# Kernel optimization log

Measured on AMD Instinct MI355X. Metric: run time of the kernel, lower is better.

## Reference

```python
import jax, jax.numpy as jnp
import numpy as np

B, QS, KS = 8, 1024, 1024
QDIM = KDIM = VDIM = 512
HEADS, ODIM = 8, 64
NEG_SLOPE = 0.2


def setup_inputs() -> dict:
    key = jax.random.key(0)
    ks = jax.random.split(key, 7)
    return {
        "Q": jax.random.normal(ks[0], (B, QS, QDIM), jnp.float32),
        "K": jax.random.normal(ks[1], (B, KS, KDIM), jnp.float32),
        "V": jax.random.normal(ks[2], (B, KS, VDIM), jnp.float32),
        # torch Linear weights: (out_features, in_features)
        "WQ": jax.random.normal(ks[3], (HEADS, QDIM), jnp.float32) * 0.05,
        "WK": jax.random.normal(ks[4], (HEADS, KDIM), jnp.float32) * 0.05,
        "WV": jax.random.normal(ks[5], (HEADS * ODIM, VDIM), jnp.float32) * 0.05,
        "bias": jax.random.normal(ks[6], (HEADS, ODIM), jnp.float32) * 0.05,
    }


def reference(Q, K, V, WQ, WK, WV, bias):
    b, qs = Q.shape[:2]
    Vproj = (V @ WV.T).reshape(b, -1, HEADS, ODIM)          # (b, k, h, d)
    attn_K = K @ WK.T                                        # (b, k, h)
    attn_Q = Q @ WQ.T                                        # (b, q, h)
    # additive GAT-style scores: (b, q, k, h)
    w = jax.nn.leaky_relu(attn_Q[:, :, None, :] + attn_K[:, None, :, :],
                          negative_slope=NEG_SLOPE)
    w = jax.nn.softmax(w, axis=2)                            # softmax over keys
    out = jnp.einsum('bqkh,bkhd->bqhd', w, Vproj) + bias     # (b, q, h, d)
    return out.reshape(b, qs, -1)
```

## Files before the change

kernel.cpp:

```cpp
#include <hip/hip_runtime.h>
#include <hip/hip_bf16.h>

#define NS 0.2f


typedef _Float16 half8 __attribute__((ext_vector_type(8)));
typedef float f32x4 __attribute__((ext_vector_type(4)));

__global__ __launch_bounds__(256) void projQK_kernel(
    const float* __restrict__ Q, const float* __restrict__ K,
    const float* __restrict__ WQ, const float* __restrict__ WK,
    float* __restrict__ aQ, float* __restrict__ aK) {
  int bid = blockIdx.x;
  const float* X;
  const float* W;
  float* aX;
  int rb;
  if (bid < 512) { X = Q; W = WQ; aX = aQ; rb = bid; }
  else           { X = K; W = WK; aX = aK; rb = bid - 512; }
  __shared__ __align__(16) float Wl[8 * 512];
  int t = threadIdx.x;
#pragma unroll
  for (int i = 0; i < 16; i++) Wl[i * 256 + t] = W[i * 256 + t];
  __syncthreads();
  int w = t >> 6, lane = t & 63;
#pragma unroll
  for (int r = 0; r < 4; r++) {
    int row = rb * 16 + w * 4 + r;
    const float* x = X + (size_t)row * 512;
    float4 x0 = *(const float4*)(x + lane * 4);
    float4 x1 = *(const float4*)(x + 256 + lane * 4);
    float acc[8];
#pragma unroll
    for (int h = 0; h < 8; h++) {
      const float* wl = Wl + h * 512;
      float4 w0 = *(const float4*)(wl + lane * 4);
      float4 w1 = *(const float4*)(wl + 256 + lane * 4);
      float a = x0.x * w0.x + x0.y * w0.y + x0.z * w0.z + x0.w * w0.w +
                x1.x * w1.x + x1.y * w1.y + x1.z * w1.z + x1.w * w1.w;
#pragma unroll
      for (int off = 32; off > 0; off >>= 1) a += __shfl_xor(a, off);
      acc[h] = a;
    }
    if (lane == 0) {
      float* o = aX + (size_t)row * 8;
      o[0] = acc[0]; o[1] = acc[1]; o[2] = acc[2]; o[3] = acc[3];
      o[4] = acc[4]; o[5] = acc[5]; o[6] = acc[6]; o[7] = acc[7];
    }
  }
}

__global__ __launch_bounds__(256) void vproj_mfma(
    const float* __restrict__ A, const float* __restrict__ Wv,
    _Float16* __restrict__ C) {
  __shared__ __align__(16) _Float16 As[64 * 64];
  __shared__ __align__(16) _Float16 Bs[64 * 64];
  int t = threadIdx.x;
  int m0 = blockIdx.x * 64, n0 = blockIdx.y * 64;
  int lane = t & 63, wid = t >> 6;
  int wr = wid >> 1, wc = wid & 1;
  int sr = t >> 2, sc = t & 3;
  const float* ap = A + (size_t)(m0 + sr) * 512 + sc * 16;
  const float* bp = Wv + (size_t)(n0 + sr) * 512 + sc * 16;
  int swz = sr & 7;
  _Float16* aw0 = As + sr * 64 + (((2 * sc + 0) ^ swz) * 8);
  _Float16* aw1 = As + sr * 64 + (((2 * sc + 1) ^ swz) * 8);
  _Float16* bw0 = Bs + sr * 64 + (((2 * sc + 0) ^ swz) * 8);
  _Float16* bw1 = Bs + sr * 64 + (((2 * sc + 1) ^ swz) * 8);
  int fr = lane & 15, fs = lane >> 4;
  f32x4 acc[2][2];
#pragma unroll
  for (int i = 0; i < 2; i++)
#pragma unroll
    for (int j = 0; j < 2; j++)
#pragma unroll
      for (int r = 0; r < 4; r++) acc[i][j][r] = 0.f;

  float4 a0 = *(const float4*)(ap);
  float4 a1 = *(const float4*)(ap + 4);
  float4 a2 = *(const float4*)(ap + 8);
  float4 a3 = *(const float4*)(ap + 12);
  float4 b0 = *(const float4*)(bp);
  float4 b1 = *(const float4*)(bp + 4);
  float4 b2 = *(const float4*)(bp + 8);
  float4 b3 = *(const float4*)(bp + 12);
  for (int k0 = 0; k0 < 512; k0 += 64) {
    half8 ah0, ah1, bh0, bh1;
    ah0[0] = (_Float16)a0.x; ah0[1] = (_Float16)a0.y;
    ah0[2] = (_Float16)a0.z; ah0[3] = (_Float16)a0.w;
    ah0[4] = (_Float16)a1.x; ah0[5] = (_Float16)a1.y;
    ah0[6] = (_Float16)a1.z; ah0[7] = (_Float16)a1.w;
    ah1[0] = (_Float16)a2.x; ah1[1] = (_Float16)a2.y;
    ah1[2] = (_Float16)a2.z; ah1[3] = (_Float16)a2.w;
    ah1[4] = (_Float16)a3.x; ah1[5] = (_Float16)a3.y;
    ah1[6] = (_Float16)a3.z; ah1[7] = (_Float16)a3.w;
    bh0[0] = (_Float16)b0.x; bh0[1] = (_Float16)b0.y;
    bh0[2] = (_Float16)b0.z; bh0[3] = (_Float16)b0.w;
    bh0[4] = (_Float16)b1.x; bh0[5] = (_Float16)b1.y;
    bh0[6] = (_Float16)b1.z; bh0[7] = (_Float16)b1.w;
    bh1[0] = (_Float16)b2.x; bh1[1] = (_Float16)b2.y;
    bh1[2] = (_Float16)b2.z; bh1[3] = (_Float16)b2.w;
    bh1[4] = (_Float16)b3.x; bh1[5] = (_Float16)b3.y;
    bh1[6] = (_Float16)b3.z; bh1[7] = (_Float16)b3.w;
    if (k0 + 64 < 512) {
      a0 = *(const float4*)(ap + k0 + 64);
      a1 = *(const float4*)(ap + k0 + 68);
      a2 = *(const float4*)(ap + k0 + 72);
      a3 = *(const float4*)(ap + k0 + 76);
      b0 = *(const float4*)(bp + k0 + 64);
      b1 = *(const float4*)(bp + k0 + 68);
      b2 = *(const float4*)(bp + k0 + 72);
      b3 = *(const float4*)(bp + k0 + 76);
    }
    __syncthreads();
    *(half8*)aw0 = ah0;
    *(half8*)aw1 = ah1;
    *(half8*)bw0 = bh0;
    *(half8*)bw1 = bh1;
    __syncthreads();
    half8 af[2][2], bf[2][2];
#pragma unroll
    for (int i = 0; i < 2; i++) {
      int R = wr * 32 + i * 16 + fr;
#pragma unroll
      for (int kk = 0; kk < 2; kk++)
        af[i][kk] = *(half8*)(As + R * 64 + (((fs + 4 * kk) ^ (R & 7)) * 8));
    }
#pragma unroll
    for (int j = 0; j < 2; j++) {
      int Cc = wc * 32 + j * 16 + fr;
#pragma unroll
      for (int kk = 0; kk < 2; kk++)
        bf[j][kk] = *(half8*)(Bs + Cc * 64 + (((fs + 4 * kk) ^ (Cc & 7)) * 8));
    }
#pragma unroll
    for (int i = 0; i < 2; i++)
#pragma unroll
      for (int j = 0; j < 2; j++) {
        acc[i][j] = __builtin_amdgcn_mfma_f32_16x16x32_f16(
            af[i][0], bf[j][0], acc[i][j], 0, 0, 0);
        acc[i][j] = __builtin_amdgcn_mfma_f32_16x16x32_f16(
            af[i][1], bf[j][1], acc[i][j], 0, 0, 0);
      }
  }
#pragma unroll
  for (int i = 0; i < 2; i++)
#pragma unroll
    for (int j = 0; j < 2; j++) {
      int row = m0 + wr * 32 + i * 16 + fs * 4;
      int col = n0 + wc * 32 + j * 16 + fr;
#pragma unroll
      for (int r = 0; r < 4; r++)
        C[(size_t)(row + r) * 512 + col] = (_Float16)acc[i][j][r];
    }
}

__global__ __launch_bounds__(1024) void sortbin_kernel(
    const float* __restrict__ aK, const float* __restrict__ aQ,
    const _Float16* __restrict__ Vp, float* __restrict__ E1g,
    float* __restrict__ E2g, int* __restrict__ IDXg,
    float* __restrict__ cofs1, float* __restrict__ cofs2,
    float* __restrict__ scof1, float* __restrict__ scof2,
    float* __restrict__ amaxArr, int* __restrict__ binStart,
    int* __restrict__ binData, float* __restrict__ binX) {
  int bh = blockIdx.x, b = bh >> 3, h = bh & 7;
  __shared__ float key[1024];
  __shared__ int idx[1024];
  __shared__ float E1s[1024], E2s[1024];
  __shared__ float ct1[32][64], ct2[32][64];
  __shared__ float sct1[32], sct2[32];
  __shared__ int cnt[32], bstart[33];
  int t = threadIdx.x;
  float k = aK[(size_t)(b * 1024 + t) * 8 + h];
  int id = t;
  for (int len = 2; len <= 1024; len <<= 1) {
    bool up = ((t & len) == 0);
    for (int stride = len >> 1; stride >= 64; stride >>= 1) {
      key[t] = k; idx[t] = id;
      __syncthreads();
      int p = t ^ stride;
      float k2 = key[p];
      int i2 = idx[p];
      __syncthreads();
      bool takeMin = (((t & stride) == 0) == up);
      bool take2 = takeMin ? (k2 < k) : (k2 > k);
      if (take2) { k = k2; id = i2; }
    }
    int s0 = (len >> 1) < 32 ? (len >> 1) : 32;
    for (int stride = s0; stride >= 1; stride >>= 1) {
      float k2 = __shfl_xor(k, stride);
      int i2 = __shfl_xor(id, stride);
      bool takeMin = (((t & stride) == 0) == up);
      bool take2 = takeMin ? (k2 < k) : (k2 > k);
      if (take2) { k = k2; id = i2; }
    }
  }
  key[t] = k; idx[t] = id;
  __syncthreads();
  float amax = key[1023];
  float e1 = __expf(k - amax);
  float e2 = __expf(NS * (k - amax));
  E1s[t] = e1; E2s[t] = e2;
  E1g[bh * 1024 + t] = e1;
  E2g[bh * 1024 + t] = e2;
  IDXg[bh * 1024 + t] = id;
  if (t == 0) amaxArr[bh] = amax;
  __syncthreads();
  {
    int d = t & 63;
    const _Float16* vb = Vp + (size_t)b * 1024 * 512 + h * 64 + d;
    for (int cc = t >> 6; cc < 32; cc += 16) {
      float t1 = 0.f, t2 = 0.f;
#pragma unroll 8
      for (int j = 0; j < 32; j++) {
        int i = cc * 32 + j;
        float v = (float)vb[(size_t)idx[i] * 512];
        t1 += E1s[i] * v;
        t2 += E2s[i] * v;
      }
      ct1[cc][d] = t1; ct2[cc][d] = t2;
    }
    if (t < 32) {
      float s1 = 0.f, s2 = 0.f;
      for (int j = 0; j < 32; j++) { s1 += E1s[t * 32 + j]; s2 += E2s[t * 32 + j]; }
      sct1[t] = s1; sct2[t] = s2;
    }
  }
  __syncthreads();
  {
    int d = t & 63;
    for (int cc = t >> 6; cc < 32; cc += 16) {
      float o1 = 0.f, o2 = 0.f;
      for (int kk = cc + 1; kk < 32; kk++) o1 += ct1[kk][d];
      for (int kk = 0; kk < cc; kk++) o2 += ct2[kk][d];
      cofs1[(bh * 32 + cc) * 64 + d] = o1;
      cofs2[(bh * 32 + cc) * 64 + d] = o2;
    }
    if (t < 32) {
      float o1 = 0.f, o2 = 0.f;
      for (int kk = t + 1; kk < 32; kk++) o1 += sct1[kk];
      for (int kk = 0; kk < t; kk++) o2 += sct2[kk];
      scof1[bh * 32 + t] = o1;
      scof2[bh * 32 + t] = o2;
    }
  }
  float x = aQ[(size_t)(b * 1024 + t) * 8 + h];
  float negx = -x;
  int lo = 0, hi = 1024;
  while (lo < hi) {
    int mid = (lo + hi) >> 1;
    if (key[mid] <= negx) lo = mid + 1; else hi = mid;
  }
  int ix = lo;
  int c = ix >> 5; if (c > 31) c = 31;
  if (t < 32) cnt[t] = 0;
  __syncthreads();
  int slot = atomicAdd(&cnt[c], 1);
  __syncthreads();
  if (t == 0) {
    int s = 0;
    for (int i = 0; i < 32; i++) { bstart[i] = s; s += cnt[i]; }
    bstart[32] = s;
  }
  __syncthreads();
  if (t < 33) binStart[bh * 33 + t] = bstart[t];
  int pos = bstart[c] + slot;
  binData[bh * 1024 + pos] = (t << 11) | ix;
  binX[bh * 1024 + pos] = x;
}

__global__ __launch_bounds__(256) void final_binned(
    const float* __restrict__ E1g, const float* __restrict__ E2g,
    const int* __restrict__ IDXg, const _Float16* __restrict__ Vp,
    const float* __restrict__ cofs1, const float* __restrict__ cofs2,
    const float* __restrict__ scof1, const float* __restrict__ scof2,
    const float* __restrict__ amaxArr, const int* __restrict__ binStart,
    const int* __restrict__ binData, const float* __restrict__ binX,
    const float* __restrict__ aQ, const float* __restrict__ bias,
    float* __restrict__ out) {
  int blk = blockIdx.x;
  int bh = blk >> 5, c = blk & 31;
  int b = bh >> 3, h = bh & 7;
  int t = threadIdx.x, w = t >> 6, lane = t & 63;
  __shared__ float P1[33][64], P2[33][64];
  __shared__ float G1s[4][64], G2s[4][64];
  __shared__ float sS1[33], sS2[33];
  __shared__ float e1c[32], e2c[32];
  int n0 = binStart[bh * 33 + c];
  int n = binStart[bh * 33 + c + 1] - n0;
  if (n == 0) return;
  if (t < 32) {
    e1c[t] = E1g[bh * 1024 + c * 32 + t];
    e2c[t] = E2g[bh * 1024 + c * 32 + t];
  }
  __syncthreads();
  float f1[8], f2[8];
  {
    const _Float16* vb = Vp + (size_t)b * 1024 * 512 + h * 64 + lane;
    const int* ib = IDXg + bh * 1024 + c * 32 + w * 8;
#pragma unroll
    for (int k2 = 0; k2 < 8; k2++) {
      float v = (float)vb[(size_t)ib[k2] * 512];
      f1[k2] = e1c[w * 8 + k2] * v;
      f2[k2] = e2c[w * 8 + k2] * v;
    }
  }
  float G1 = 0.f, G2 = 0.f;
#pragma unroll
  for (int k2 = 0; k2 < 8; k2++) { G1 += f1[k2]; G2 += f2[k2]; }
  G1s[w][lane] = G1;
  G2s[w][lane] = G2;
  if (t == 0) {
    float s = 0.f;
    sS1[32] = 0.f;
    for (int l = 31; l >= 0; l--) { s += e1c[l]; sS1[l] = s; }
    s = 0.f;
    sS2[0] = 0.f;
    for (int l = 1; l <= 32; l++) { s += e2c[l - 1]; sS2[l] = s; }
  }
  __syncthreads();
  float off1 = 0.f, off2 = 0.f;
#pragma unroll
  for (int w2 = 0; w2 < 4; w2++) {
    float g1 = G1s[w2][lane], g2 = G2s[w2][lane];
    if (w2 > w) off1 += g1;
    if (w2 < w) off2 += g2;
  }
  {
    float p1v[8];
    float s = 0.f;
#pragma unroll
    for (int k2 = 7; k2 >= 0; k2--) { s += f1[k2]; p1v[k2] = s; }
#pragma unroll
    for (int k2 = 0; k2 < 8; k2++) P1[w * 8 + k2][lane] = off1 + p1v[k2];
    float p = 0.f;
#pragma unroll
    for (int k2 = 0; k2 < 8; k2++) { P2[w * 8 + k2][lane] = off2 + p; p += f2[k2]; }
    if (w == 3) P2[32][lane] = off2 + p;
    if (w == 0) P1[32][lane] = 0.f;
  }
  float o1 = cofs1[(bh * 32 + c) * 64 + lane];
  float o2 = cofs2[(bh * 32 + c) * 64 + lane];
  float so1 = scof1[bh * 32 + c];
  float so2 = scof2[bh * 32 + c];
  float amax = amaxArr[bh];
  float bi = bias[h * 64 + lane];
  __syncthreads();
  for (int qi = w; qi < n; qi += 4) {
    int rec = binData[bh * 1024 + n0 + qi];
    float x = binX[bh * 1024 + n0 + qi];
    int q = rec >> 11;
    int l = (rec & 2047) - c * 32;
    float num1 = o1 + P1[l][lane];
    float num2 = o2 + P2[l][lane];
    float xs = x + amax;
    float ex = __expf(xs), e2x = __expf(NS * xs);
    float Z = ex * (so1 + sS1[l]) + e2x * (so2 + sS2[l]);
    out[((size_t)(b * 1024 + q)) * 512 + h * 64 + lane] =
        (ex * num1 + e2x * num2) / Z + bi;
  }
}

__global__ __launch_bounds__(256) void vproj_gemm(
    const float* __restrict__ A, const float* __restrict__ Wv,
    float* __restrict__ C) {
  __shared__ __align__(16) float As[16][68];
  __shared__ __align__(16) float Bs[16][68];
  int t = threadIdx.x;
  int m0 = blockIdx.x * 64, n0 = blockIdx.y * 64;
  int tx = t & 15, ty = t >> 4;
  int lr = t >> 2, lk = (t & 3) * 4;
  float acc[4][4] = {{0.f}};
  const float* ap = A + (size_t)(m0 + lr) * 512 + lk;
  const float* bp = Wv + (size_t)(n0 + lr) * 512 + lk;
  for (int k0 = 0; k0 < 512; k0 += 16) {
    float4 av = *(const float4*)(ap + k0);
    float4 bv = *(const float4*)(bp + k0);
    __syncthreads();
    As[lk + 0][lr] = av.x; As[lk + 1][lr] = av.y;
    As[lk + 2][lr] = av.z; As[lk + 3][lr] = av.w;
    Bs[lk + 0][lr] = bv.x; Bs[lk + 1][lr] = bv.y;
    Bs[lk + 2][lr] = bv.z; Bs[lk + 3][lr] = bv.w;
    __syncthreads();
#pragma unroll
    for (int kk = 0; kk < 16; kk++) {
      float4 a4 = *(const float4*)&As[kk][ty * 4];
      float4 b4 = *(const float4*)&Bs[kk][tx * 4];
      float aa[4] = {a4.x, a4.y, a4.z, a4.w};
      float bb[4] = {b4.x, b4.y, b4.z, b4.w};
#pragma unroll
      for (int i = 0; i < 4; i++)
#pragma unroll
        for (int j = 0; j < 4; j++) acc[i][j] += aa[i] * bb[j];
    }
  }
#pragma unroll
  for (int i = 0; i < 4; i++) {
    float4 o = {acc[i][0], acc[i][1], acc[i][2], acc[i][3]};
    *(float4*)(C + (size_t)(m0 + ty * 4 + i) * 512 + n0 + tx * 4) = o;
  }
}

__global__ __launch_bounds__(256) void direct_kernel(
    const float* __restrict__ aQ, const float* __restrict__ aK,
    const float* __restrict__ Vp, const float* __restrict__ bias,
    float* __restrict__ out) {
  int id = blockIdx.x;
  int qt = id & 15, h = (id >> 4) & 7, b = id >> 7;
  __shared__ float AK[1024], E1s[1024], E2s[1024];
  __shared__ __align__(16) float VT[128][64];
  __shared__ float XQ[64];
  int t = threadIdx.x;
  for (int i = t; i < 1024; i += 256) {
    float a = aK[(size_t)(b * 1024 + i) * 8 + h];
    AK[i] = a; E1s[i] = __expf(a); E2s[i] = __expf(NS * a);
  }
  if (t < 64) XQ[t] = aQ[(size_t)(b * 1024 + qt * 64 + t) * 8 + h];
  __syncthreads();
  int w = t >> 6, d = t & 63;
  float xq[16], ex[16], e2x[16], acc[16], z[16];
#pragma unroll
  for (int qi = 0; qi < 16; qi++) {
    float x = XQ[w * 16 + qi];
    xq[qi] = x; ex[qi] = __expf(x); e2x[qi] = __expf(NS * x);
    acc[qi] = 0.f; z[qi] = 0.f;
  }
  for (int kt = 0; kt < 8; kt++) {
    __syncthreads();
    for (int i = t; i < 128 * 64; i += 256) {
      VT[i >> 6][i & 63] =
          Vp[(size_t)(b * 1024 + kt * 128 + (i >> 6)) * 512 + h * 64 + (i & 63)];
    }
    __syncthreads();
    for (int kk = 0; kk < 128; kk++) {
      int k = kt * 128 + kk;
      float a = AK[k], e1 = E1s[k], e2 = E2s[k];
      float v = VT[kk][d];
#pragma unroll
      for (int qi = 0; qi < 16; qi++) {
        float wsel = (a + xq[qi] > 0.f) ? (ex[qi] * e1) : (e2x[qi] * e2);
        acc[qi] += wsel * v;
        z[qi] += wsel;
      }
    }
  }
#pragma unroll
  for (int qi = 0; qi < 16; qi++) {
    int q = qt * 64 + w * 16 + qi;
    out[(size_t)(b * 1024 + q) * 512 + h * 64 + d] =
        acc[qi] / z[qi] + bias[h * 64 + d];
  }
}

__global__ __launch_bounds__(256) void projQK_fb_kernel(
    const float* __restrict__ Q, const float* __restrict__ K,
    const float* __restrict__ WQ, const float* __restrict__ WK,
    float* __restrict__ aQ, float* __restrict__ aK) {
  int bid = blockIdx.x;
  const float* X;
  const float* W;
  float* aX;
  int rb;
  if (bid < 512) { X = Q; W = WQ; aX = aQ; rb = bid; }
  else           { X = K; W = WK; aX = aK; rb = bid - 512; }
  __shared__ __align__(16) float Wl[8 * 512];
  int t = threadIdx.x;
#pragma unroll
  for (int i = 0; i < 16; i++) Wl[i * 256 + t] = W[i * 256 + t];
  __syncthreads();
  int w = t >> 6, lane = t & 63;
#pragma unroll
  for (int r = 0; r < 4; r++) {
    int row = rb * 16 + w * 4 + r;
    const float* x = X + (size_t)row * 512;
    float4 x0 = *(const float4*)(x + lane * 4);
    float4 x1 = *(const float4*)(x + 256 + lane * 4);
    float acc[8];
#pragma unroll
    for (int h = 0; h < 8; h++) {
      const float* wl = Wl + h * 512;
      float4 w0 = *(const float4*)(wl + lane * 4);
      float4 w1 = *(const float4*)(wl + 256 + lane * 4);
      float a = x0.x * w0.x + x0.y * w0.y + x0.z * w0.z + x0.w * w0.w +
                x1.x * w1.x + x1.y * w1.y + x1.z * w1.z + x1.w * w1.w;
#pragma unroll
      for (int off = 32; off > 0; off >>= 1) a += __shfl_xor(a, off);
      acc[h] = a;
    }
    if (lane == 0) {
      float* o = aX + (size_t)row * 8;
      o[0] = acc[0]; o[1] = acc[1]; o[2] = acc[2]; o[3] = acc[3];
      o[4] = acc[4]; o[5] = acc[5]; o[6] = acc[6]; o[7] = acc[7];
    }
  }
}

extern "C" void kernel_launch(void* const* d_in, const int* in_sizes, int n_in,
                              void* d_out, int out_size, void* d_ws,
                              size_t ws_size, hipStream_t stream) {
  const float* Q = (const float*)d_in[0];
  const float* K = (const float*)d_in[1];
  const float* V = (const float*)d_in[2];
  const float* WQ = (const float*)d_in[3];
  const float* WK = (const float*)d_in[4];
  const float* WV = (const float*)d_in[5];
  const float* bias = (const float*)d_in[6];
  float* out = (float*)d_out;
  char* ws = (char*)d_ws;

  const size_t oAQ   = 0;
  const size_t oAK   = 262144;
  const size_t oE1   = 524288;
  const size_t oE2   = 786432;
  const size_t oIDX  = 1048576;
  const size_t oCOF1 = 1310720;
  const size_t oCOF2 = 1835008;
  const size_t oSC1  = 2359296;
  const size_t oSC2  = 2375680;
  const size_t oAMX  = 2392064;
  const size_t oBST  = 2396160;
  const size_t oBDA  = 2412544;
  const size_t oBX   = 2674688;
  const size_t oVP   = 2936832;
  const size_t NEED_MAIN = oVP + 8388608;
  const size_t NEED_FB = 524288 + 16777216;

  if (ws_size >= NEED_MAIN) {
    float* aQ = (float*)(ws + oAQ);
    float* aK = (float*)(ws + oAK);
    float* E1g = (float*)(ws + oE1);
    float* E2g = (float*)(ws + oE2);
    int* IDXg = (int*)(ws + oIDX);
    float* cofs1 = (float*)(ws + oCOF1);
    float* cofs2 = (float*)(ws + oCOF2);
    float* scof1 = (float*)(ws + oSC1);
    float* scof2 = (float*)(ws + oSC2);
    float* amaxA = (float*)(ws + oAMX);
    int* binSt = (int*)(ws + oBST);
    int* binDa = (int*)(ws + oBDA);
    float* binX = (float*)(ws + oBX);
    _Float16* Vp = (_Float16*)(ws + oVP);
    hipLaunchKernelGGL(projQK_kernel, dim3(1024), dim3(256), 0, stream, Q, K,
                       WQ, WK, aQ, aK);
    hipLaunchKernelGGL(vproj_mfma, dim3(128, 8), dim3(256), 0, stream, V, WV,
                       Vp);
    hipLaunchKernelGGL(sortbin_kernel, dim3(64), dim3(1024), 0, stream, aK, aQ,
                       Vp, E1g, E2g, IDXg, cofs1, cofs2, scof1, scof2, amaxA,
                       binSt, binDa, binX);
    hipLaunchKernelGGL(final_binned, dim3(2048), dim3(256), 0, stream, E1g,
                       E2g, IDXg, Vp, cofs1, cofs2, scof1, scof2, amaxA, binSt,
                       binDa, binX, aQ, bias, out);
  } else if (ws_size >= NEED_FB) {
    float* aQ = (float*)(ws + 0);
    float* aK = (float*)(ws + 262144);
    float* Vpf = (float*)(ws + 524288);
    hipLaunchKernelGGL(projQK_fb_kernel, dim3(1024), dim3(256), 0, stream, Q,
                       K, WQ, WK, aQ, aK);
    hipLaunchKernelGGL(vproj_gemm, dim3(128, 8), dim3(256), 0, stream, V, WV,
                       Vpf);
    hipLaunchKernelGGL(direct_kernel, dim3(1024), dim3(256), 0, stream, aQ, aK,
                       Vpf, bias, out);
  }
}
```

Baseline: 72.42 us.

## Split chunk-total computation out of sort kernel and pre-convert V to fp16

The per-chunk weighted V totals and the prefix/suffix offsets move out of the 64-block sort kernel. A new 512-block kernel computes the chunk totals, and the final kernel rebuilds the offsets itself. The aim is to stop a 64-block kernel from serialising gather-heavy work. Separately, V and WV are converted to fp16 by a standalone kernel so the GEMM loads halves directly. This adds an extra pass over V, extra workspace and an extra launch, and the final kernel now does redundant summation per block.

```diff
diff --git a/kernel.cpp b/kernel.cpp
--- a/kernel.cpp
+++ b/kernel.cpp
@@ -50,8 +50,28 @@
   }
 }
 
-__global__ __launch_bounds__(256) void vproj_mfma(
-    const float* __restrict__ A, const float* __restrict__ Wv,
+__global__ __launch_bounds__(256) void convert_kernel(
+    const float* __restrict__ V, const float* __restrict__ WV,
+    _Float16* __restrict__ Vh, _Float16* __restrict__ WVh) {
+  const size_t n1 = (size_t)8192 * 512;
+  size_t i = ((size_t)blockIdx.x * 256 + threadIdx.x) * 8;
+  const float* src;
+  _Float16* dst;
+  size_t j;
+  if (i < n1) { src = V; dst = Vh; j = i; }
+  else        { src = WV; dst = WVh; j = i - n1; }
+  float4 a = *(const float4*)(src + j);
+  float4 b = *(const float4*)(src + j + 4);
+  half8 h;
+  h[0] = (_Float16)a.x; h[1] = (_Float16)a.y;
+  h[2] = (_Float16)a.z; h[3] = (_Float16)a.w;
+  h[4] = (_Float16)b.x; h[5] = (_Float16)b.y;
+  h[6] = (_Float16)b.z; h[7] = (_Float16)b.w;
+  *(half8*)(dst + j) = h;
+}
+
+__global__ __launch_bounds__(256) void gemm_f16(
+    const _Float16* __restrict__ A, const _Float16* __restrict__ B,
     _Float16* __restrict__ C) {
   __shared__ __align__(16) _Float16 As[64 * 64];
   __shared__ __align__(16) _Float16 Bs[64 * 64];
@@ -59,14 +79,14 @@
   int m0 = blockIdx.x * 64, n0 = blockIdx.y * 64;
   int lane = t & 63, wid = t >> 6;
   int wr = wid >> 1, wc = wid & 1;
-  int sr = t >> 2, sc = t & 3;
-  const float* ap = A + (size_t)(m0 + sr) * 512 + sc * 16;
-  const float* bp = Wv + (size_t)(n0 + sr) * 512 + sc * 16;
+  int sr = t >> 2, sq = t & 3;
   int swz = sr & 7;
-  _Float16* aw0 = As + sr * 64 + (((2 * sc + 0) ^ swz) * 8);
-  _Float16* aw1 = As + sr * 64 + (((2 * sc + 1) ^ swz) * 8);
-  _Float16* bw0 = Bs + sr * 64 + (((2 * sc + 0) ^ swz) * 8);
-  _Float16* bw1 = Bs + sr * 64 + (((2 * sc + 1) ^ swz) * 8);
+  const _Float16* ap = A + (size_t)(m0 + sr) * 512;
+  const _Float16* bp = B + (size_t)(n0 + sr) * 512;
+  int g0 = (2 * sq) ^ swz;
+  int g1 = (2 * sq + 1) ^ swz;
+  _Float16* awr = As + sr * 64 + 2 * sq * 8;
+  _Float16* bwr = Bs + sr * 64 + 2 * sq * 8;
   int fr = lane & 15, fs = lane >> 4;
   f32x4 acc[2][2];
 #pragma unroll
@@ -76,47 +96,22 @@
 #pragma unroll
       for (int r = 0; r < 4; r++) acc[i][j][r] = 0.f;
 
-  float4 a0 = *(const float4*)(ap);
-  float4 a1 = *(const float4*)(ap + 4);
-  float4 a2 = *(const float4*)(ap + 8);
-  float4 a3 = *(const float4*)(ap + 12);
-  float4 b0 = *(const float4*)(bp);
-  float4 b1 = *(const float4*)(bp + 4);
-  float4 b2 = *(const float4*)(bp + 8);
-  float4 b3 = *(const float4*)(bp + 12);
+  uint4 va0 = *(const uint4*)(ap + g0 * 8);
+  uint4 va1 = *(const uint4*)(ap + g1 * 8);
+  uint4 vb0 = *(const uint4*)(bp + g0 * 8);
+  uint4 vb1 = *(const uint4*)(bp + g1 * 8);
   for (int k0 = 0; k0 < 512; k0 += 64) {
-    half8 ah0, ah1, bh0, bh1;
-    ah0[0] = (_Float16)a0.x; ah0[1] = (_Float16)a0.y;
-    ah0[2] = (_Float16)a0.z; ah0[3] = (_Float16)a0.w;
-    ah0[4] = (_Float16)a1.x; ah0[5] = (_Float16)a1.y;
-    ah0[6] = (_Float16)a1.z; ah0[7] = (_Float16)a1.w;
-    ah1[0] = (_Float16)a2.x; ah1[1] = (_Float16)a2.y;
-    ah1[2] = (_Float16)a2.z; ah1[3] = (_Float16)a2.w;
-    ah1[4] = (_Float16)a3.x; ah1[5] = (_Float16)a3.y;
-    ah1[6] = (_Float16)a3.z; ah1[7] = (_Float16)a3.w;
-    bh0[0] = (_Float16)b0.x; bh0[1] = (_Float16)b0.y;
-    bh0[2] = (_Float16)b0.z; bh0[3] = (_Float16)b0.w;
-    bh0[4] = (_Float16)b1.x; bh0[5] = (_Float16)b1.y;
-    bh0[6] = (_Float16)b1.z; bh0[7] = (_Float16)b1.w;
-    bh1[0] = (_Float16)b2.x; bh1[1] = (_Float16)b2.y;
-    bh1[2] = (_Float16)b2.z; bh1[3] = (_Float16)b2.w;
-    bh1[4] = (_Float16)b3.x; bh1[5] = (_Float16)b3.y;
-    bh1[6] = (_Float16)b3.z; bh1[7] = (_Float16)b3.w;
+    __syncthreads();
+    *(uint4*)awr = va0;
+    *(uint4*)(awr + 8) = va1;
+    *(uint4*)bwr = vb0;
+    *(uint4*)(bwr + 8) = vb1;
     if (k0 + 64 < 512) {
-      a0 = *(const float4*)(ap + k0 + 64);
-      a1 = *(const float4*)(ap + k0 + 68);
-      a2 = *(const float4*)(ap + k0 + 72);
-      a3 = *(const float4*)(ap + k0 + 76);
-      b0 = *(const float4*)(bp + k0 + 64);
-      b1 = *(const float4*)(bp + k0 + 68);
-      b2 = *(const float4*)(bp + k0 + 72);
-      b3 = *(const float4*)(bp + k0 + 76);
-    }
-    __syncthreads();
-    *(half8*)aw0 = ah0;
-    *(half8*)aw1 = ah1;
-    *(half8*)bw0 = bh0;
-    *(half8*)bw1 = bh1;
+      va0 = *(const uint4*)(ap + k0 + 64 + g0 * 8);
+      va1 = *(const uint4*)(ap + k0 + 64 + g1 * 8);
+      vb0 = *(const uint4*)(bp + k0 + 64 + g0 * 8);
+      vb1 = *(const uint4*)(bp + k0 + 64 + g1 * 8);
+    }
     __syncthreads();
     half8 af[2][2], bf[2][2];
 #pragma unroll
@@ -157,18 +152,12 @@
 
 __global__ __launch_bounds__(1024) void sortbin_kernel(
     const float* __restrict__ aK, const float* __restrict__ aQ,
-    const _Float16* __restrict__ Vp, float* __restrict__ E1g,
-    float* __restrict__ E2g, int* __restrict__ IDXg,
-    float* __restrict__ cofs1, float* __restrict__ cofs2,
-    float* __restrict__ scof1, float* __restrict__ scof2,
+    float* __restrict__ E1g, float* __restrict__ E2g, int* __restrict__ IDXg,
     float* __restrict__ amaxArr, int* __restrict__ binStart,
     int* __restrict__ binData, float* __restrict__ binX) {
   int bh = blockIdx.x, b = bh >> 3, h = bh & 7;
   __shared__ float key[1024];
   __shared__ int idx[1024];
-  __shared__ float E1s[1024], E2s[1024];
-  __shared__ float ct1[32][64], ct2[32][64];
-  __shared__ float sct1[32], sct2[32];
   __shared__ int cnt[32], bstart[33];
   int t = threadIdx.x;
   float k = aK[(size_t)(b * 1024 + t) * 8 + h];
@@ -198,52 +187,10 @@
   key[t] = k; idx[t] = id;
   __syncthreads();
   float amax = key[1023];
-  float e1 = __expf(k - amax);
-  float e2 = __expf(NS * (k - amax));
-  E1s[t] = e1; E2s[t] = e2;
-  E1g[bh * 1024 + t] = e1;
-  E2g[bh * 1024 + t] = e2;
+  E1g[bh * 1024 + t] = __expf(k - amax);
+  E2g[bh * 1024 + t] = __expf(NS * (k - amax));
   IDXg[bh * 1024 + t] = id;
   if (t == 0) amaxArr[bh] = amax;
-  __syncthreads();
-  {
-    int d = t & 63;
-    const _Float16* vb = Vp + (size_t)b * 1024 * 512 + h * 64 + d;
-    for (int cc = t >> 6; cc < 32; cc += 16) {
-      float t1 = 0.f, t2 = 0.f;
-#pragma unroll 8
-      for (int j = 0; j < 32; j++) {
-        int i = cc * 32 + j;
-        float v = (float)vb[(size_t)idx[i] * 512];
-        t1 += E1s[i] * v;
-        t2 += E2s[i] * v;
-      }
-      ct1[cc][d] = t1; ct2[cc][d] = t2;
-    }
-    if (t < 32) {
-      float s1 = 0.f, s2 = 0.f;
-      for (int j = 0; j < 32; j++) { s1 += E1s[t * 32 + j]; s2 += E2s[t * 32 + j]; }
-      sct1[t] = s1; sct2[t] = s2;
-    }
-  }
-  __syncthreads();
-  {
-    int d = t & 63;
-    for (int cc = t >> 6; cc < 32; cc += 16) {
-      float o1 = 0.f, o2 = 0.f;
-      for (int kk = cc + 1; kk < 32; kk++) o1 += ct1[kk][d];
-      for (int kk = 0; kk < cc; kk++) o2 += ct2[kk][d];
-      cofs1[(bh * 32 + cc) * 64 + d] = o1;
-      cofs2[(bh * 32 + cc) * 64 + d] = o2;
-    }
-    if (t < 32) {
-      float o1 = 0.f, o2 = 0.f;
-      for (int kk = t + 1; kk < 32; kk++) o1 += sct1[kk];
-      for (int kk = 0; kk < t; kk++) o2 += sct2[kk];
-      scof1[bh * 32 + t] = o1;
-      scof2[bh * 32 + t] = o2;
-    }
-  }
   float x = aQ[(size_t)(b * 1024 + t) * 8 + h];
   float negx = -x;
   int lo = 0, hi = 1024;
@@ -269,15 +216,49 @@
   binX[bh * 1024 + pos] = x;
 }
 
+__global__ __launch_bounds__(256) void ctot_kernel(
+    const float* __restrict__ E1g, const float* __restrict__ E2g,
+    const int* __restrict__ IDXg, const _Float16* __restrict__ Vp,
+    float* __restrict__ ct1, float* __restrict__ ct2,
+    float* __restrict__ sct1, float* __restrict__ sct2) {
+  int blk = blockIdx.x;
+  int bh = blk >> 3, g = blk & 7;
+  int b = bh >> 3, h = bh & 7;
+  __shared__ float E1[128], E2[128];
+  __shared__ int IDX[128];
+  int t = threadIdx.x;
+  if (t < 128) {
+    int gi = bh * 1024 + g * 128 + t;
+    E1[t] = E1g[gi];
+    E2[t] = E2g[gi];
+    IDX[t] = IDXg[gi];
+  }
+  __syncthreads();
+  int c = t >> 6, d = t & 63;
+  const _Float16* vb = Vp + (size_t)b * 1024 * 512 + h * 64 + d;
+  float t1 = 0.f, t2 = 0.f, s1 = 0.f, s2 = 0.f;
+#pragma unroll 8
+  for (int j = 0; j < 32; j++) {
+    int il = c * 32 + j;
+    float v = (float)vb[(size_t)IDX[il] * 512];
+    float e1 = E1[il], e2 = E2[il];
+    t1 += e1 * v; t2 += e2 * v;
+    s1 += e1; s2 += e2;
+  }
+  int cc = g * 4 + c;
+  ct1[(bh * 32 + cc) * 64 + d] = t1;
+  ct2[(bh * 32 + cc) * 64 + d] = t2;
+  if (d == 0) { sct1[bh * 32 + cc] = s1; sct2[bh * 32 + cc] = s2; }
+}
+
 __global__ __launch_bounds__(256) void final_binned(
     const float* __restrict__ E1g, const float* __restrict__ E2g,
     const int* __restrict__ IDXg, const _Float16* __restrict__ Vp,
-    const float* __restrict__ cofs1, const float* __restrict__ cofs2,
-    const float* __restrict__ scof1, const float* __restrict__ scof2,
+    const float* __restrict__ ct1, const float* __restrict__ ct2,
+    const float* __restrict__ sct1, const float* __restrict__ sct2,
     const float* __restrict__ amaxArr, const int* __restrict__ binStart,
     const int* __restrict__ binData, const float* __restrict__ binX,
-    const float* __restrict__ aQ, const float* __restrict__ bias,
-    float* __restrict__ out) {
+    const float* __restrict__ bias, float* __restrict__ out) {
   int blk = blockIdx.x;
   int bh = blk >> 5, c = blk & 31;
   int b = bh >> 3, h = bh & 7;
@@ -286,12 +267,33 @@
   __shared__ float G1s[4][64], G2s[4][64];
   __shared__ float sS1[33], sS2[33];
   __shared__ float e1c[32], e2c[32];
+  __shared__ float cofsL1[64], cofsL2[64];
+  __shared__ float soL[2];
   int n0 = binStart[bh * 33 + c];
   int n = binStart[bh * 33 + c + 1] - n0;
   if (n == 0) return;
   if (t < 32) {
     e1c[t] = E1g[bh * 1024 + c * 32 + t];
     e2c[t] = E2g[bh * 1024 + c * 32 + t];
+  }
+  if (t < 64) {
+    float o1 = 0.f, o2 = 0.f;
+#pragma unroll
+    for (int k = 0; k < 32; k++) {
+      float v1 = ct1[(bh * 32 + k) * 64 + t];
+      float v2 = ct2[(bh * 32 + k) * 64 + t];
+      if (k > c) o1 += v1;
+      if (k < c) o2 += v2;
+    }
+    cofsL1[t] = o1; cofsL2[t] = o2;
+  } else if (t == 64) {
+    float s = 0.f;
+    for (int k = c + 1; k < 32; k++) s += sct1[bh * 32 + k];
+    soL[0] = s;
+  } else if (t == 65) {
+    float s = 0.f;
+    for (int k = 0; k < c; k++) s += sct2[bh * 32 + k];
+    soL[1] = s;
   }
   __syncthreads();
   float f1[8], f2[8];
@@ -339,10 +341,10 @@
     if (w == 3) P2[32][lane] = off2 + p;
     if (w == 0) P1[32][lane] = 0.f;
   }
-  float o1 = cofs1[(bh * 32 + c) * 64 + lane];
-  float o2 = cofs2[(bh * 32 + c) * 64 + lane];
-  float so1 = scof1[bh * 32 + c];
-  float so2 = scof2[bh * 32 + c];
+  float o1 = cofsL1[lane];
+  float o2 = cofsL2[lane];
+  float so1 = soL[0];
+  float so2 = soL[1];
   float amax = amaxArr[bh];
   float bi = bias[h * 64 + lane];
   __syncthreads();
@@ -513,8 +515,8 @@
   const size_t oE1   = 524288;
   const size_t oE2   = 786432;
   const size_t oIDX  = 1048576;
-  const size_t oCOF1 = 1310720;
-  const size_t oCOF2 = 1835008;
+  const size_t oCT1  = 1310720;
+  const size_t oCT2  = 1835008;
   const size_t oSC1  = 2359296;
   const size_t oSC2  = 2375680;
   const size_t oAMX  = 2392064;
@@ -522,7 +524,9 @@
   const size_t oBDA  = 2412544;
   const size_t oBX   = 2674688;
   const size_t oVP   = 2936832;
-  const size_t NEED_MAIN = oVP + 8388608;
+  const size_t oVH   = oVP + 8388608;
+  const size_t oWVH  = oVH + 8388608;
+  const size_t NEED_MAIN = oWVH + 524288;
   const size_t NEED_FB = 524288 + 16777216;
 
   if (ws_size >= NEED_MAIN) {
@@ -531,25 +535,30 @@
     float* E1g = (float*)(ws + oE1);
     float* E2g = (float*)(ws + oE2);
     int* IDXg = (int*)(ws + oIDX);
-    float* cofs1 = (float*)(ws + oCOF1);
-    float* cofs2 = (float*)(ws + oCOF2);
-    float* scof1 = (float*)(ws + oSC1);
-    float* scof2 = (float*)(ws + oSC2);
+    float* ct1 = (float*)(ws + oCT1);
+    float* ct2 = (float*)(ws + oCT2);
+    float* sct1 = (float*)(ws + oSC1);
+    float* sct2 = (float*)(ws + oSC2);
     float* amaxA = (float*)(ws + oAMX);
     int* binSt = (int*)(ws + oBST);
     int* binDa = (int*)(ws + oBDA);
     float* binX = (float*)(ws + oBX);
     _Float16* Vp = (_Float16*)(ws + oVP);
+    _Float16* Vh = (_Float16*)(ws + oVH);
+    _Float16* WVh = (_Float16*)(ws + oWVH);
     hipLaunchKernelGGL(projQK_kernel, dim3(1024), dim3(256), 0, stream, Q, K,
                        WQ, WK, aQ, aK);
-    hipLaunchKernelGGL(vproj_mfma, dim3(128, 8), dim3(256), 0, stream, V, WV,
+    hipLaunchKernelGGL(convert_kernel, dim3(2176), dim3(256), 0, stream, V,
+                       WV, Vh, WVh);
+    hipLaunchKernelGGL(gemm_f16, dim3(128, 8), dim3(256), 0, stream, Vh, WVh,
                        Vp);
-    hipLaunchKernelGGL(sortbin_kernel, dim3(64), dim3(1024), 0, stream, aK, aQ,
-                       Vp, E1g, E2g, IDXg, cofs1, cofs2, scof1, scof2, amaxA,
-                       binSt, binDa, binX);
+    hipLaunchKernelGGL(sortbin_kernel, dim3(64), dim3(1024), 0, stream, aK,
+                       aQ, E1g, E2g, IDXg, amaxA, binSt, binDa, binX);
+    hipLaunchKernelGGL(ctot_kernel, dim3(512), dim3(256), 0, stream, E1g, E2g,
+                       IDXg, Vp, ct1, ct2, sct1, sct2);
     hipLaunchKernelGGL(final_binned, dim3(2048), dim3(256), 0, stream, E1g,
-                       E2g, IDXg, Vp, cofs1, cofs2, scof1, scof2, amaxA, binSt,
-                       binDa, binX, aQ, bias, out);
+                       E2g, IDXg, Vp, ct1, ct2, sct1, sct2, amaxA, binSt,
+                       binDa, binX, bias, out);
   } else if (ws_size >= NEED_FB) {
     float* aQ = (float*)(ws + 0);
     float* aK = (float*)(ws + 262144);
```

New measurement: 66.61 us, median of 2. 1.09x faster.
